# Performance work log

Measured on AMD Instinct MI355X. Metric: run time of the kernel, lower is better.

The kernel has to match this reference:

```python
import jax, jax.numpy as jnp
import numpy as np

D_MODEL = 1024
NUM_HEADS = 16
D_K = D_MODEL // NUM_HEADS
B, S = 4, 2048
NEG = -1e9


def setup_inputs() -> dict:
    key = jax.random.key(0)
    ks = jax.random.split(key, 12)
    def lin(kw, kb):
        bound = 1.0 / np.sqrt(D_MODEL)
        W = jax.random.uniform(kw, (D_MODEL, D_MODEL), jnp.float32, -bound, bound)
        b = jax.random.uniform(kb, (D_MODEL,), jnp.float32, -bound, bound)
        return W, b
    Wq, bq = lin(ks[0], ks[1])
    Wk, bk = lin(ks[2], ks[3])
    Wv, bv = lin(ks[4], ks[5])
    Wo, bo = lin(ks[6], ks[7])
    Q = jax.random.normal(ks[8], (B, S, D_MODEL), jnp.float32)
    K = jax.random.normal(ks[9], (B, S, D_MODEL), jnp.float32)
    V = jax.random.normal(ks[10], (B, S, D_MODEL), jnp.float32)
    # causal mask: 1 = keep, 0 = masked
    mask = jnp.tril(jnp.ones((S, S), jnp.int32))[None, None, :, :]
    mask = jnp.broadcast_to(mask, (B, 1, S, S))
    return {"Q": Q, "K": K, "V": V, "mask": mask,
            "Wq": Wq, "bq": bq, "Wk": Wk, "bk": bk,
            "Wv": Wv, "bv": bv, "Wo": Wo, "bo": bo}


def _split_heads(x):
    b, s, _ = x.shape
    return x.reshape(b, s, NUM_HEADS, D_K).transpose(0, 2, 1, 3)  # [B,H,S,Dk]


def reference(Q, K, V, mask, Wq, bq, Wk, bk, Wv, bv, Wo, bo):
    q = _split_heads(Q @ Wq.T + bq)
    k = _split_heads(K @ Wk.T + bk)
    v = _split_heads(V @ Wv.T + bv)
    scores = jnp.einsum('bhqd,bhkd->bhqk', q, k) / jnp.sqrt(jnp.float32(D_K))
    scores = jnp.where(mask == 0, jnp.float32(NEG), scores)
    probs = jax.nn.softmax(scores, axis=-1)
    attn = jnp.einsum('bhqk,bhkd->bhqd', probs, v)  # [B,H,S,Dk]
    attn = attn.transpose(0, 2, 1, 3).reshape(Q.shape[0], Q.shape[1], D_MODEL)
    return attn @ Wo.T + bo
```

## Files before the change

### kernel.cpp

```cpp
#include <hip/hip_runtime.h>
#include <hip/hip_bf16.h>
#include <cstdint>

typedef float floatx4 __attribute__((ext_vector_type(4)));
typedef __bf16 bf16x8 __attribute__((ext_vector_type(8)));

#define AS_G __attribute__((address_space(1)))
#define AS_L __attribute__((address_space(3)))

__device__ __forceinline__ void async_cp16(const void* g, void* l) {
    __builtin_amdgcn_global_load_lds((const AS_G uint32_t*)g, (AS_L uint32_t*)l, 16, 0, 0);
}

__device__ __forceinline__ floatx4 mfma16x16x32(bf16x8 a, bf16x8 b, floatx4 c) {
    return __builtin_amdgcn_mfma_f32_16x16x32_bf16(a, b, c, 0, 0, 0);
}

__device__ __forceinline__ unsigned short f2bf(float x) {
    return __builtin_bit_cast(unsigned short, (__bf16)x);
}

__global__ __launch_bounds__(256) void cvt_f32_bf16(const float* __restrict__ in,
                                                    unsigned short* __restrict__ out, int n) {
    int i = (blockIdx.x * 256 + threadIdx.x) * 4;
    if (i >= n) return;
    float4 v = *(const float4*)(in + i);
    ushort4 o;
    o.x = f2bf(v.x); o.y = f2bf(v.y); o.z = f2bf(v.z); o.w = f2bf(v.w);
    *(ushort4*)(out + i) = o;
}

__global__ __launch_bounds__(256) void cvt4_f32_bf16(const float* __restrict__ a, const float* __restrict__ b,
                                                     const float* __restrict__ c, const float* __restrict__ d,
                                                     unsigned short* __restrict__ out, int n) {
    const float* in = blockIdx.y == 0 ? a : blockIdx.y == 1 ? b : blockIdx.y == 2 ? c : d;
    unsigned short* o = out + (size_t)blockIdx.y * n;
    int i = (blockIdx.x * 256 + threadIdx.x) * 4;
    if (i >= n) return;
    float4 v = *(const float4*)(in + i);
    ushort4 u;
    u.x = f2bf(v.x); u.y = f2bf(v.y); u.z = f2bf(v.z); u.w = f2bf(v.w);
    *(ushort4*)(o + i) = u;
}

template <int MODE>
__global__ __launch_bounds__(256) void gemm_bt(const unsigned short* __restrict__ A,
                                               const unsigned short* __restrict__ W,
                                               const float* __restrict__ bias,
                                               float oscale,
                                               void* __restrict__ outv) {
    __shared__ unsigned short As[128 * 64];
    __shared__ unsigned short Bs[128 * 64];
    const int tid  = threadIdx.x;
    const int wave = tid >> 6, lane = tid & 63;
    const int quad = lane >> 4, l15 = lane & 15;
    const int l7   = l15 & 7;
    const int m0 = blockIdx.x * 128, n0 = blockIdx.y * 128;
    const int waveM = (wave >> 1) * 64, waveN = (wave & 1) * 64;

    floatx4 acc[4][4] = {};

    const int r8  = lane >> 3;
    const int gsw = (lane & 7) ^ r8;

    for (int k0 = 0; k0 < 1024; k0 += 64) {
        for (int c = wave; c < 16; c += 4) {
            const int row = c * 8 + r8;
            async_cp16(A + (size_t)(m0 + row) * 1024 + k0 + gsw * 8, (char*)As + c * 1024);
            async_cp16(W + (size_t)(n0 + row) * 1024 + k0 + gsw * 8, (char*)Bs + c * 1024);
        }
        __syncthreads();

#pragma unroll
        for (int h = 0; h < 2; ++h) {
            const int g = (quad + h * 4) ^ l7;
            bf16x8 af[4], bf[4];
#pragma unroll
            for (int t = 0; t < 4; ++t) {
                af[t] = *(const bf16x8*)&As[(waveM + t * 16 + l15) * 64 + g * 8];
                bf[t] = *(const bf16x8*)&Bs[(waveN + t * 16 + l15) * 64 + g * 8];
            }
#pragma unroll
            for (int mt = 0; mt < 4; ++mt)
#pragma unroll
                for (int nt = 0; nt < 4; ++nt)
                    acc[mt][nt] = mfma16x16x32(af[mt], bf[nt], acc[mt][nt]);
        }
        __syncthreads();
    }

#pragma unroll
    for (int mt = 0; mt < 4; ++mt) {
#pragma unroll
        for (int nt = 0; nt < 4; ++nt) {
            const int gcol = n0 + waveN + nt * 16 + l15;
            const float bv = bias[gcol];
#pragma unroll
            for (int r = 0; r < 4; ++r) {
                const int grow = m0 + waveM + mt * 16 + quad * 4 + r;
                const float val = (acc[mt][nt][r] + bv) * oscale;
                if (MODE == 2) {
                    ((float*)outv)[(size_t)grow * 1024 + gcol] = val;
                } else {
                    const int b = grow >> 11, s = grow & 2047;
                    const int h = gcol >> 6, dk = gcol & 63;
                    size_t idx;
                    if (MODE == 0) idx = ((size_t)(b * 16 + h) * 2048 + s) * 64 + dk;
                    else           idx = ((size_t)(b * 16 + h) * 64 + dk) * 2048 + s;
                    ((unsigned short*)outv)[idx] = f2bf(val);
                }
            }
        }
    }
}

#define PS_STRIDE 72

template <bool DIAG>
__device__ __forceinline__ void tile_compute(const bf16x8 kf[4][2], const bf16x8 vf[2][4],
                                             unsigned short* __restrict__ Psw,
                                             bf16x8 qf0, bf16x8 qf1,
                                             int quad, int l15,
                                             int qrow0, int kv0,
                                             float* __restrict__ lsum,
                                             floatx4* __restrict__ O) {
    floatx4 sc[4];
    __builtin_amdgcn_s_setprio(1);
#pragma unroll
    for (int kvt = 0; kvt < 4; ++kvt) {
        floatx4 a = {};
        a = mfma16x16x32(qf0, kf[kvt][0], a);
        a = mfma16x16x32(qf1, kf[kvt][1], a);
        sc[kvt] = a;
    }
    __builtin_amdgcn_s_setprio(0);

#pragma unroll
    for (int kvt = 0; kvt < 4; ++kvt) {
#pragma unroll
        for (int r = 0; r < 4; ++r) {
            float s = sc[kvt][r];
            if (DIAG && (kv0 + kvt * 16 + l15 > qrow0 + r)) s = -1.0e9f;
            const float p = __builtin_amdgcn_exp2f(s);
            lsum[r] += p;
            Psw[(quad * 4 + r) * PS_STRIDE + kvt * 16 + l15] = f2bf(p);
        }
    }

    __builtin_amdgcn_s_setprio(1);
#pragma unroll
    for (int half = 0; half < 2; ++half) {
        bf16x8 pf = *(const bf16x8*)&Psw[l15 * PS_STRIDE + half * 32 + quad * 8];
#pragma unroll
        for (int nt = 0; nt < 4; ++nt)
            O[nt] = mfma16x16x32(pf, vf[half][nt], O[nt]);
    }
    __builtin_amdgcn_s_setprio(0);
}

__global__ __launch_bounds__(256, 3) void flash_causal(const unsigned short* __restrict__ qp,
                                                       const unsigned short* __restrict__ kp,
                                                       const unsigned short* __restrict__ vt,
                                                       unsigned short* __restrict__ attn) {
    __shared__ unsigned short Ks[2][64 * 64];
    __shared__ unsigned short Vs[2][64 * 64];
    __shared__ unsigned short Ps[4 * 16 * PS_STRIDE];

    const int tid  = threadIdx.x;
    const int wave = tid >> 6, lane = tid & 63;
    const int quad = lane >> 4, l15 = lane & 15;
    const int l7   = l15 & 7;
    const int bh = blockIdx.x;
    const int pr = blockIdx.y;
    const int tA = pr, tB = 31 - pr;

    unsigned short* Psw = &Ps[wave * 16 * PS_STRIDE];

    bf16x8 qfA0, qfA1, qfB0, qfB1;
    {
        const unsigned short* qa = qp + ((size_t)bh * 2048 + tA * 64 + wave * 16 + l15) * 64;
        qfA0 = *(const bf16x8*)(qa + quad * 8);
        qfA1 = *(const bf16x8*)(qa + 32 + quad * 8);
        const unsigned short* qb = qp + ((size_t)bh * 2048 + tB * 64 + wave * 16 + l15) * 64;
        qfB0 = *(const bf16x8*)(qb + quad * 8);
        qfB1 = *(const bf16x8*)(qb + 32 + quad * 8);
    }

    float lsumA[4] = {}, lsumB[4] = {};
    floatx4 OA[4] = {}, OB[4] = {};

    const int qrowA = tA * 64 + wave * 16 + quad * 4;
    const int qrowB = tB * 64 + wave * 16 + quad * 4;

    const int r8  = lane >> 3;
    const int gsw = (lane & 7) ^ r8;
    const size_t kb = (size_t)bh * 131072;
    const size_t vb = (size_t)bh * 64 * 2048;

#define STAGE(t, b) do {                                                                  \
        const int kv0_ = (t) * 64;                                                        \
        for (int c = wave; c < 8; c += 4) {                                               \
            const int row_ = c * 8 + r8;                                                  \
            async_cp16(kp + kb + (size_t)(kv0_ + row_) * 64 + gsw * 8,                    \
                       (char*)Ks[b] + c * 1024);                                          \
            async_cp16(vt + vb + (size_t)row_ * 2048 + kv0_ + gsw * 8,                    \
                       (char*)Vs[b] + c * 1024);                                          \
        } } while (0)

    STAGE(0, 0);

    int buf = 0;
    for (int t = 0; t <= tB; ++t) {
        if (t < tB) {
            STAGE(t + 1, buf ^ 1);
            asm volatile("s_waitcnt vmcnt(4)" ::: "memory");
        } else {
            asm volatile("s_waitcnt vmcnt(0)" ::: "memory");
        }
        __builtin_amdgcn_s_barrier();
        __builtin_amdgcn_sched_barrier(0);

        const unsigned short* Kc = Ks[buf];
        const unsigned short* Vc = Vs[buf];

        bf16x8 kf[4][2], vf[2][4];
        const int g1 = quad ^ l7, g2 = (quad + 4) ^ l7;
#pragma unroll
        for (int kvt = 0; kvt < 4; ++kvt) {
            kf[kvt][0] = *(const bf16x8*)&Kc[(kvt * 16 + l15) * 64 + g1 * 8];
            kf[kvt][1] = *(const bf16x8*)&Kc[(kvt * 16 + l15) * 64 + g2 * 8];
        }
#pragma unroll
        for (int half = 0; half < 2; ++half) {
            const int gb = (quad + half * 4) ^ l7;
#pragma unroll
            for (int nt = 0; nt < 4; ++nt)
                vf[half][nt] = *(const bf16x8*)&Vc[(nt * 16 + l15) * 64 + gb * 8];
        }

        const int kv0 = t * 64;
        if (t == tB) tile_compute<true >(kf, vf, Psw, qfB0, qfB1, quad, l15, qrowB, kv0, lsumB, OB);
        else         tile_compute<false>(kf, vf, Psw, qfB0, qfB1, quad, l15, qrowB, kv0, lsumB, OB);
        if (t == tA)      tile_compute<true >(kf, vf, Psw, qfA0, qfA1, quad, l15, qrowA, kv0, lsumA, OA);
        else if (t < tA)  tile_compute<false>(kf, vf, Psw, qfA0, qfA1, quad, l15, qrowA, kv0, lsumA, OA);

        asm volatile("s_waitcnt lgkmcnt(0)" ::: "memory");
        __builtin_amdgcn_sched_barrier(0);
        __builtin_amdgcn_s_barrier();
        buf ^= 1;
    }
#undef STAGE

    const int b = bh >> 4, h = bh & 15;
#pragma unroll
    for (int r = 0; r < 4; ++r) {
        float lA = lsumA[r], lB = lsumB[r];
#pragma unroll
        for (int off = 8; off; off >>= 1) {
            lA += __shfl_xor(lA, off, 16);
            lB += __shfl_xor(lB, off, 16);
        }
        const float invA = 1.0f / lA;
        const float invB = 1.0f / lB;
        const size_t rbA = ((size_t)b * 2048 + qrowA + r) * 1024 + h * 64;
        const size_t rbB = ((size_t)b * 2048 + qrowB + r) * 1024 + h * 64;
#pragma unroll
        for (int nt = 0; nt < 4; ++nt) {
            attn[rbA + nt * 16 + l15] = f2bf(OA[nt][r] * invA);
            attn[rbB + nt * 16 + l15] = f2bf(OB[nt][r] * invB);
        }
    }
}

extern "C" void kernel_launch(void* const* d_in, const int* in_sizes, int n_in,
                              void* d_out, int out_size, void* d_ws, size_t ws_size,
                              hipStream_t stream) {
    const float* Q  = (const float*)d_in[0];
    const float* K  = (const float*)d_in[1];
    const float* V  = (const float*)d_in[2];
    const float* Wq = (const float*)d_in[4];  const float* bq = (const float*)d_in[5];
    const float* Wk = (const float*)d_in[6];  const float* bk = (const float*)d_in[7];
    const float* Wv = (const float*)d_in[8];  const float* bv = (const float*)d_in[9];
    const float* Wo = (const float*)d_in[10]; const float* bo = (const float*)d_in[11];
    float* out = (float*)d_out;

    const int NIN = 8192 * 1024;
    const int NW  = 1024 * 1024;

    unsigned short* ws   = (unsigned short*)d_ws;
    unsigned short* inb  = ws;
    unsigned short* wb   = inb + NIN;
    unsigned short* qp   = wb + 4 * NW;
    unsigned short* kp   = qp + NIN;
    unsigned short* vtp  = kp + NIN;
    unsigned short* attnb = vtp + NIN;

    const float QSCL = 0.125f * 1.44269504088896f;

    dim3 blk(256);
    dim3 gcvtW((NW + 1023) / 1024, 4);
    dim3 gcvtA((NIN + 1023) / 1024);
    dim3 ggemm(64, 8);
    dim3 gflash(64, 16);

    cvt4_f32_bf16<<<gcvtW, blk, 0, stream>>>(Wq, Wk, Wv, Wo, wb, NW);

    cvt_f32_bf16<<<gcvtA, blk, 0, stream>>>(Q, inb, NIN);
    gemm_bt<0><<<ggemm, blk, 0, stream>>>(inb, wb + 0 * NW, bq, QSCL, (void*)qp);
    cvt_f32_bf16<<<gcvtA, blk, 0, stream>>>(K, inb, NIN);
    gemm_bt<0><<<ggemm, blk, 0, stream>>>(inb, wb + 1 * NW, bk, 1.0f, (void*)kp);
    cvt_f32_bf16<<<gcvtA, blk, 0, stream>>>(V, inb, NIN);
    gemm_bt<1><<<ggemm, blk, 0, stream>>>(inb, wb + 2 * NW, bv, 1.0f, (void*)vtp);

    flash_causal<<<gflash, blk, 0, stream>>>(qp, kp, vtp, attnb);

    gemm_bt<2><<<ggemm, blk, 0, stream>>>(attnb, wb + 3 * NW, bo, 1.0f, (void*)out);
}
```

Measured before the change: 363.3 us.

## Double-buffer GEMM LDS tiles with async prefetch of next k-slice

Converts the projection GEMM's single LDS tile into two buffers and issues the global-to-LDS copies for the next k-step before computing on the current one. Explicit vmcnt waits and raw barriers replace __syncthreads so the loads overlap the MFMA work. LDS use doubles to 64KB per block, with a launch bound of 2 blocks per CU. The hand-set vmcnt(8) assumes exactly 8 outstanding loads per wave, which is fragile if the loop structure changes.

After: 365.3 us. About the same (+0.6%).

```diff
diff --git a/kernel.cpp b/kernel.cpp
--- a/kernel.cpp
+++ b/kernel.cpp
@@ -44,13 +44,13 @@
 }
 
 template <int MODE>
-__global__ __launch_bounds__(256) void gemm_bt(const unsigned short* __restrict__ A,
-                                               const unsigned short* __restrict__ W,
-                                               const float* __restrict__ bias,
-                                               float oscale,
-                                               void* __restrict__ outv) {
-    __shared__ unsigned short As[128 * 64];
-    __shared__ unsigned short Bs[128 * 64];
+__global__ __launch_bounds__(256, 2) void gemm_bt(const unsigned short* __restrict__ A,
+                                                  const unsigned short* __restrict__ W,
+                                                  const float* __restrict__ bias,
+                                                  float oscale,
+                                                  void* __restrict__ outv) {
+    __shared__ unsigned short As[2][128 * 64];
+    __shared__ unsigned short Bs[2][128 * 64];
     const int tid  = threadIdx.x;
     const int wave = tid >> 6, lane = tid & 63;
     const int quad = lane >> 4, l15 = lane & 15;
@@ -63,13 +63,30 @@
     const int r8  = lane >> 3;
     const int gsw = (lane & 7) ^ r8;
 
+#define GSTAGE(k0_, b_) do {                                                              \
+        for (int c = wave; c < 16; c += 4) {                                              \
+            const int row_ = c * 8 + r8;                                                  \
+            async_cp16(A + (size_t)(m0 + row_) * 1024 + (k0_) + gsw * 8,                  \
+                       (char*)As[b_] + c * 1024);                                         \
+            async_cp16(W + (size_t)(n0 + row_) * 1024 + (k0_) + gsw * 8,                  \
+                       (char*)Bs[b_] + c * 1024);                                         \
+        } } while (0)
+
+    GSTAGE(0, 0);
+
+    int buf = 0;
     for (int k0 = 0; k0 < 1024; k0 += 64) {
-        for (int c = wave; c < 16; c += 4) {
-            const int row = c * 8 + r8;
-            async_cp16(A + (size_t)(m0 + row) * 1024 + k0 + gsw * 8, (char*)As + c * 1024);
-            async_cp16(W + (size_t)(n0 + row) * 1024 + k0 + gsw * 8, (char*)Bs + c * 1024);
-        }
-        __syncthreads();
+        if (k0 < 960) {
+            GSTAGE(k0 + 64, buf ^ 1);
+            asm volatile("s_waitcnt vmcnt(8)" ::: "memory");
+        } else {
+            asm volatile("s_waitcnt vmcnt(0)" ::: "memory");
+        }
+        __builtin_amdgcn_s_barrier();
+        __builtin_amdgcn_sched_barrier(0);
+
+        const unsigned short* Ac = As[buf];
+        const unsigned short* Bc = Bs[buf];
 
 #pragma unroll
         for (int h = 0; h < 2; ++h) {
@@ -77,8 +94,8 @@
             bf16x8 af[4], bf[4];
 #pragma unroll
             for (int t = 0; t < 4; ++t) {
-                af[t] = *(const bf16x8*)&As[(waveM + t * 16 + l15) * 64 + g * 8];
-                bf[t] = *(const bf16x8*)&Bs[(waveN + t * 16 + l15) * 64 + g * 8];
+                af[t] = *(const bf16x8*)&Ac[(waveM + t * 16 + l15) * 64 + g * 8];
+                bf[t] = *(const bf16x8*)&Bc[(waveN + t * 16 + l15) * 64 + g * 8];
             }
 #pragma unroll
             for (int mt = 0; mt < 4; ++mt)
@@ -86,8 +103,13 @@
                 for (int nt = 0; nt < 4; ++nt)
                     acc[mt][nt] = mfma16x16x32(af[mt], bf[nt], acc[mt][nt]);
         }
-        __syncthreads();
-    }
+
+        asm volatile("s_waitcnt lgkmcnt(0)" ::: "memory");
+        __builtin_amdgcn_sched_barrier(0);
+        __builtin_amdgcn_s_barrier();
+        buf ^= 1;
+    }
+#undef GSTAGE
 
 #pragma unroll
     for (int mt = 0; mt < 4; ++mt) {
```
